# Kernel tuning notes

Measured on AMD Instinct MI355X. Metric: run time of the kernel, lower is better.

Reference implementation:

```python
import jax, jax.numpy as jnp
import numpy as np
from jax import lax

D = 256; NH = 8; LYR = 2; G = 64; K = G * G; T = 4; EC = 32
B = 4; N = 512; CITY = 256; DFF = 4 * D

def _conv(x, w):
    return lax.conv_general_dilated(x, w, (1, 1), 'SAME', dimension_numbers=('NCHW', 'OIHW', 'NCHW'))

def _ln(x, w, b):
    m = x.mean(-1, keepdims=True)
    v = ((x - m) ** 2).mean(-1, keepdims=True)
    return (x - m) / jnp.sqrt(v + 1e-5) * w + b

def _mlp(x, w1, b1, w2, b2):
    return jax.nn.gelu(x @ w1 + b1) @ w2 + b2

def setup_inputs():
    key = jax.random.key(0)
    ks = iter(jax.random.split(key, 64))
    def nrm(shape, s=0.02):
        return jax.random.normal(next(ks), shape, jnp.float32) * s
    return {
        'meas_xy': jax.random.uniform(next(ks), (B, N, 2), jnp.float32),
        'meas_v': jax.random.normal(next(ks), (B, N), jnp.float32),
        'bs_xy': jax.random.uniform(next(ks), (B, 1, 2), jnp.float32),
        'task_id': jax.random.randint(next(ks), (B,), 0, T),
        'city': jax.random.uniform(next(ks), (B, CITY, CITY), jnp.float32),
        'mp_w1': nrm((3, D)), 'mp_b1': jnp.zeros((D,)), 'mp_w2': nrm((D, D)), 'mp_b2': jnp.zeros((D,)),
        'bp_w1': nrm((2, D)), 'bp_b1': jnp.zeros((D,)), 'bp_w2': nrm((D, D)), 'bp_b2': jnp.zeros((D,)),
        'env_w1': nrm((EC, 1, 3, 3)), 'env_b1': jnp.zeros((EC,)),
        'env_w2': nrm((EC, EC, 3, 3)), 'env_b2': jnp.zeros((EC,)),
        'env_w3': nrm((D, EC, 1, 1)), 'env_b3': jnp.zeros((D,)),
        'task_emb': nrm((T, D)), 'tp_w': nrm((D, D)), 'tp_b': jnp.zeros((D,)),
        'grid_pos': nrm((K, D)),
        'blk_dens_w': nrm((LYR, D)), 'blk_dens_b': jnp.zeros((LYR, D)),
        'blk_ln1_w': jnp.ones((LYR, D)), 'blk_ln1_b': jnp.zeros((LYR, D)),
        'blk_wq': nrm((LYR, D, D)), 'blk_bq': jnp.zeros((LYR, D)),
        'blk_wk': nrm((LYR, D, D)), 'blk_bk': jnp.zeros((LYR, D)),
        'blk_wv': nrm((LYR, D, D)), 'blk_bv': jnp.zeros((LYR, D)),
        'blk_wo': nrm((LYR, D, D)), 'blk_bo': jnp.zeros((LYR, D)),
        'blk_ln2_w': jnp.ones((LYR, D)), 'blk_ln2_b': jnp.zeros((LYR, D)),
        'blk_ff_w1': nrm((LYR, D, DFF)), 'blk_ff_b1': jnp.zeros((LYR, DFF)),
        'blk_ff_w2': nrm((LYR, DFF, D)), 'blk_ff_b2': jnp.zeros((LYR, D)),
        'tfp_w': nrm((T, D, D)), 'tfp_b': jnp.zeros((T, D)),
        'head_w': nrm((D, 1)), 'head_b': jnp.zeros((1,)),
    }

def reference(meas_xy, meas_v, bs_xy, task_id, city, mp_w1, mp_b1, mp_w2, mp_b2, bp_w1, bp_b1, bp_w2, bp_b2, env_w1, env_b1, env_w2, env_b2, env_w3, env_b3, task_emb, tp_w, tp_b, grid_pos, blk_dens_w, blk_dens_b, blk_ln1_w, blk_ln1_b, blk_wq, blk_bq, blk_wk, blk_bk, blk_wv, blk_bv, blk_wo, blk_bo, blk_ln2_w, blk_ln2_b, blk_ff_w1, blk_ff_b1, blk_ff_w2, blk_ff_b2, tfp_w, tfp_b, head_w, head_b):
    b = meas_xy.shape[0]
    dh = D // NH
    # normalized grid cell centers, [K,2] in (x,y) order
    c = (jnp.arange(G, dtype=jnp.float32) + 0.5) / G
    gy, gx = jnp.meshgrid(c, c, indexing='ij')
    grid_xy = jnp.stack([gx, gy], -1).reshape(K, 2)
    meas_tok = _mlp(jnp.concatenate([meas_xy, meas_v[..., None]], -1), mp_w1, mp_b1, mp_w2, mp_b2)
    bs_tok = _mlp(bs_xy, bp_w1, bp_b1, bp_w2, bp_b2)
    src = jnp.concatenate([meas_tok, bs_tok], 1)       # [B,Ns,D]
    src_xy = jnp.concatenate([meas_xy, bs_xy], 1)      # [B,Ns,2]
    # distance bias: [B,K,Ns]
    attn_bias = -jnp.linalg.norm(grid_xy[None, :, None, :] - src_xy[:, None, :, :], axis=-1)
    # gaussian measurement density: [B,K]
    diff = grid_xy[None, :, None, :] - meas_xy[:, None, :, :]
    dist2 = (diff * diff).sum(-1)
    sigma = 0.08
    density = jnp.exp(-dist2 / (2.0 * sigma * sigma)).mean(-1)
    # env branch: nearest-resize city to GxG, small CNN
    idx = jnp.floor(jnp.arange(G) * (city.shape[1] / G)).astype(jnp.int32)
    city_grid = city[:, idx][:, :, idx][:, None]       # [B,1,G,G]
    h = jax.nn.gelu(_conv(city_grid, env_w1) + env_b1[None, :, None, None])
    h = jax.nn.gelu(_conv(h, env_w2) + env_b2[None, :, None, None])
    env_map = _conv(h, env_w3) + env_b3[None, :, None, None]
    env_grid = env_map.transpose(0, 2, 3, 1).reshape(b, K, D)
    task_vec = (task_emb[task_id] @ tp_w + tp_b)[:, None, :]
    grid = grid_pos[None] + task_vec + env_grid
    inv_sqrt = jnp.float32(1.0 / np.sqrt(dh))
    for l in range(LYR):
        # density modulation injected into the grid latent
        g = grid + density[..., None] * blk_dens_w[l] + blk_dens_b[l]
        hn = _ln(g, blk_ln1_w[l], blk_ln1_b[l])
        q = (hn @ blk_wq[l] + blk_bq[l]).reshape(b, K, NH, dh)
        kk = (src @ blk_wk[l] + blk_bk[l]).reshape(b, -1, NH, dh)
        vv = (src @ blk_wv[l] + blk_bv[l]).reshape(b, -1, NH, dh)
        scores = jnp.einsum('bkhd,bnhd->bhkn', q, kk) * inv_sqrt + attn_bias[:, None]
        a = jax.nn.softmax(scores, -1)
        o = jnp.einsum('bhkn,bnhd->bkhd', a, vv).reshape(b, K, D) @ blk_wo[l] + blk_bo[l]
        g = g + o
        g = g + _mlp(_ln(g, blk_ln2_w[l], blk_ln2_b[l]), blk_ff_w1[l], blk_ff_b1[l], blk_ff_w2[l], blk_ff_b2[l])
        grid = g
    # per-sample task projection from the weight bank
    tf = jax.nn.gelu(jnp.einsum('bkd,bdh->bkh', grid, tfp_w[task_id]) + tfp_b[task_id][:, None, :])
    logits = (tf @ head_w + head_b)[..., 0].reshape(b, G, G)
    return logits
```

## Files before the change

### kernel.cpp

```cpp
#include <hip/hip_runtime.h>
#include <hip/hip_bf16.h>
#include <math.h>

#define D 256
#define NH 8
#define DH 32
#define LYR 2
#define G 64
#define KK 4096
#define T 4
#define EC 32
#define B 4
#define N 512
#define CITY 256
#define DFF 1024
#define NS 513
#define NSP 544
#define MSRC 2052
#define MSRCP 2176
#define ISQ 0.17677669529663687f
#define LOG2E 1.4426950408889634f

typedef short bf16x8 __attribute__((ext_vector_type(8)));
typedef float f32x4 __attribute__((ext_vector_type(4)));

__device__ __forceinline__ float gelu_f(float x) {
    const float c2 = 2.f * 0.7978845608028654f * LOG2E;
    float u = x + 0.044715f * x * x * x;
    float e = __builtin_amdgcn_exp2f(-c2 * u);
    return x * __builtin_amdgcn_rcpf(1.f + e);
}

__device__ __forceinline__ unsigned short f2bf(float f) {
    unsigned int u = __float_as_uint(f);
    unsigned int r = (u + 0x7FFFu + ((u >> 16) & 1u)) >> 16;
    return (unsigned short)r;
}

__device__ __forceinline__ float bf2f(unsigned short u) {
    return __uint_as_float((unsigned)u << 16);
}

__device__ __forceinline__ unsigned cvtpk(float a, float b) {
    unsigned r;
    asm("v_cvt_pk_bf16_f32 %0, %1, %2" : "=v"(r) : "v"(a), "v"(b));
    return r;
}

__device__ __forceinline__ void gl2lds16(const unsigned short* g, unsigned short* l) {
    __builtin_amdgcn_global_load_lds(
        (const __attribute__((address_space(1))) unsigned int*)g,
        (__attribute__((address_space(3))) unsigned int*)l, 16, 0, 0);
}

__global__ __launch_bounds__(256) void pre1_k(
    const float* __restrict__ wq, const float* __restrict__ wk,
    const float* __restrict__ wv, const float* __restrict__ wo,
    const float* __restrict__ ff1, const float* __restrict__ ff2,
    const float* __restrict__ tfp,
    const float* __restrict__ bk, const float* __restrict__ bv,
    unsigned short* __restrict__ wqT, unsigned short* __restrict__ kvT,
    unsigned short* __restrict__ woT, unsigned short* __restrict__ ff1T,
    unsigned short* __restrict__ ff2T, unsigned short* __restrict__ tfpT,
    float* __restrict__ kvbias,
    const float* __restrict__ meas_xy, const float* __restrict__ meas_v,
    const float* __restrict__ bs_xy,
    const float* __restrict__ mp_w1, const float* __restrict__ mp_b1,
    const float* __restrict__ mp_w2, const float* __restrict__ mp_b2,
    const float* __restrict__ bp_w1, const float* __restrict__ bp_b1,
    const float* __restrict__ bp_w2, const float* __restrict__ bp_b2,
    unsigned short* __restrict__ srcbf, float* __restrict__ src_xy,
    float* __restrict__ dens,
    const float* __restrict__ city, const float* __restrict__ env_w1,
    const float* __restrict__ env_b1, float* __restrict__ h1,
    const float* __restrict__ task_emb, const int* __restrict__ task_id,
    const float* __restrict__ tp_w, const float* __restrict__ tp_b,
    float* __restrict__ tvec,
    unsigned short* __restrict__ khd, unsigned short* __restrict__ vch)
{
    __shared__ float sh[1088];
    int bx = blockIdx.x;
    int tid = threadIdx.x;
    if (bx < 1792) {
        const float* src; unsigned short* dst;
        int Kd, Nn, nmat, rowOff = 0, t; size_t matStride;
        if (bx < 512) {
            int job = bx >> 7; t = bx & 127;
            Kd = 256; Nn = 256; nmat = 2;
            if (job == 0)      { src = wq; dst = wqT; matStride = 65536; }
            else if (job == 1) { src = wk; dst = kvT; matStride = 131072; }
            else if (job == 2) { src = wv; dst = kvT; matStride = 131072; rowOff = 256; }
            else               { src = wo; dst = woT; matStride = 65536; }
            if ((t & 63) == 0 && job == 1) kvbias[(t >> 6) * 512 + tid] = bk[(t >> 6) * 256 + tid];
            if ((t & 63) == 0 && job == 2) kvbias[(t >> 6) * 512 + 256 + tid] = bv[(t >> 6) * 256 + tid];
        } else if (bx < 1024) { t = bx - 512;  src = ff1; dst = ff1T; Kd = 256;  Nn = 1024; nmat = 2; matStride = 262144; }
        else if (bx < 1536)   { t = bx - 1024; src = ff2; dst = ff2T; Kd = 1024; Nn = 256;  nmat = 2; matStride = 262144; }
        else                  { t = bx - 1536; src = tfp; dst = tfpT; Kd = 256;  Nn = 256;  nmat = 4; matStride = 65536; }
        int tn = Nn / 32, perMat = tn * (Kd / 32);
        int mat = t / perMat;
        int rem = t - mat * perMat;
        int nb = (rem % tn) * 32, kb = (rem / tn) * 32;
        const float* s = src + (size_t)mat * Kd * Nn;
        unsigned short* d = dst + (size_t)mat * matStride;
        float (*tb)[33] = (float (*)[33])sh;
        int tx = tid & 31, ty = tid >> 5;
        #pragma unroll
        for (int i = 0; i < 4; i++)
            tb[ty + i * 8][tx] = s[(size_t)(kb + ty + i * 8) * Nn + nb + tx];
        __syncthreads();
        #pragma unroll
        for (int i = 0; i < 4; i++)
            d[(size_t)(rowOff + nb + ty + i * 8) * Kd + kb + tx] = f2bf(tb[tx][ty + i * 8]);
    } else if (bx < 3968) {
        int id = bx - 1792;
        int dd = tid;
        if (id >= B * N + B) {
            srcbf[(size_t)id * D + dd] = 0;
            return;
        }
        float* hid = sh;
        int row;
        const float *w1, *b1, *w2, *b2;
        float x0, x1, x2 = 0.f;
        int nin;
        if (id < B * N) {
            int b = id >> 9, n = id & 511;
            x0 = meas_xy[(b * N + n) * 2 + 0];
            x1 = meas_xy[(b * N + n) * 2 + 1];
            x2 = meas_v[b * N + n];
            w1 = mp_w1; b1 = mp_b1; w2 = mp_w2; b2 = mp_b2; nin = 3;
            row = b * NS + n;
        } else {
            int b = id - B * N;
            x0 = bs_xy[b * 2 + 0];
            x1 = bs_xy[b * 2 + 1];
            w1 = bp_w1; b1 = bp_b1; w2 = bp_w2; b2 = bp_b2; nin = 2;
            row = b * NS + N;
        }
        float h = x0 * w1[dd] + x1 * w1[D + dd] + b1[dd];
        if (nin == 3) h += x2 * w1[2 * D + dd];
        hid[dd] = gelu_f(h);
        __syncthreads();
        float o = b2[dd];
        for (int j = 0; j < D; j++) o += hid[j] * w2[j * D + dd];
        srcbf[(size_t)row * D + dd] = f2bf(o);
        if (dd == 0) { src_xy[row * 2 + 0] = x0; src_xy[row * 2 + 1] = x1; }
    } else if (bx < 4032) {
        int blk = bx - 3968;
        int b = blk >> 4, kc = blk & 15;
        int k = kc * 256 + tid;
        float* mx = sh; float* my = sh + 512;
        for (int i = tid; i < N; i += 256) {
            mx[i] = meas_xy[(b * N + i) * 2 + 0];
            my[i] = meas_xy[(b * N + i) * 2 + 1];
        }
        __syncthreads();
        float gx = ((k & 63) + 0.5f) / 64.f;
        float gy = ((k >> 6) + 0.5f) / 64.f;
        float s = 0.f;
        for (int n = 0; n < N; n++) {
            float dx = gx - mx[n], dy = gy - my[n];
            s += __expf(-(dx * dx + dy * dy) * 78.125f);
        }
        dens[b * KK + k] = s * (1.f / (float)N);
    } else if (bx < 6080) {
        int i = (bx - 4032) * 256 + tid;
        int x = i & 63, y = (i >> 6) & 63, c = (i >> 12) & 31, b = i >> 17;
        float s = env_b1[c];
        for (int ky = 0; ky < 3; ky++) {
            int yy = y + ky - 1;
            if (yy < 0 || yy >= G) continue;
            for (int kx = 0; kx < 3; kx++) {
                int xx = x + kx - 1;
                if (xx < 0 || xx >= G) continue;
                s += city[(b * CITY + yy * 4) * CITY + xx * 4] * env_w1[c * 9 + ky * 3 + kx];
            }
        }
        h1[i] = gelu_f(s);
    } else if (bx < 6084) {
        int b = bx - 6080;
        float* e = sh;
        e[tid] = task_emb[task_id[b] * D + tid];
        __syncthreads();
        float s = tp_b[tid];
        for (int j = 0; j < D; j++) s += e[j] * tp_w[j * D + tid];
        tvec[b * D + tid] = s;
    } else {
        int bh = bx - 6084;
        unsigned short* kp = khd + ((size_t)bh * 544 + 513) * 32;
        for (int i = tid; i < 992; i += 256) kp[i] = 0;
        unsigned short* vp = vch + ((size_t)bh * 17 + 16) * 1024;
        for (int i = tid; i < 1024; i += 256) vp[i] = 0;
    }
}

__global__ __launch_bounds__(256) void conv2_k(
    const float* __restrict__ h1, const float* __restrict__ w,
    const float* __restrict__ bias, float* __restrict__ h2) {
    int blk = blockIdx.x;
    int yt = blk & 15, cg = (blk >> 4) & 7, b = blk >> 7;
    int x = threadIdx.x & 63, y = yt * 4 + (threadIdx.x >> 6);
    int c0 = cg * 4;
    float flag[9];
    int off[9];
    #pragma unroll
    for (int ky = 0; ky < 3; ky++) {
        int yy = y + ky - 1;
        bool vy = (yy >= 0 && yy < G);
        int yc = min(max(yy, 0), G - 1);
        #pragma unroll
        for (int kx = 0; kx < 3; kx++) {
            int xx = x + kx - 1;
            bool vx = (xx >= 0 && xx < G);
            int xc = min(max(xx, 0), G - 1);
            flag[ky * 3 + kx] = (vy && vx) ? 1.f : 0.f;
            off[ky * 3 + kx] = yc * G + xc;
        }
    }
    const float* hp = h1 + ((size_t)(b * EC) << 12);
    float acc[4] = {bias[c0], bias[c0 + 1], bias[c0 + 2], bias[c0 + 3]};
    float v[9], nv[9];
    #pragma unroll
    for (int t = 0; t < 9; t++) v[t] = hp[off[t]] * flag[t];
    for (int ci = 0; ci < EC; ci++) {
        if (ci < EC - 1) {
            const float* hn = hp + ((size_t)(ci + 1) << 12);
            #pragma unroll
            for (int t = 0; t < 9; t++) nv[t] = hn[off[t]] * flag[t];
        }
        #pragma unroll
        for (int cc = 0; cc < 4; cc++) {
            const float* wp = w + ((size_t)(c0 + cc) * EC + ci) * 9;
            #pragma unroll
            for (int t = 0; t < 9; t++) acc[cc] += v[t] * wp[t];
        }
        #pragma unroll
        for (int t = 0; t < 9; t++) v[t] = nv[t];
    }
    size_t obase = (((size_t)(b * EC + c0)) << 12) + y * G + x;
    #pragma unroll
    for (int cc = 0; cc < 4; cc++)
        h2[obase + ((size_t)cc << 12)] = gelu_f(acc[cc]);
}

__global__ __launch_bounds__(256) void pre2_k(
    const float* __restrict__ h2, const float* __restrict__ w3,
    const float* __restrict__ b3, const float* __restrict__ grid_pos,
    const float* __restrict__ tvec, float* __restrict__ grid,
    float* __restrict__ out, const float* __restrict__ head_b)
{
    __shared__ float sh[1088];
    int bx = blockIdx.x;
    int tid = threadIdx.x;
    if (bx < 2048) {
        int b = bx >> 9, k0 = (bx & 511) * 8;
        float (*h2s)[8] = (float (*)[8])sh;
        h2s[tid >> 3][tid & 7] = h2[(((size_t)b * EC + (tid >> 3)) << 12) + k0 + (tid & 7)];
        float w3r[32];
        #pragma unroll
        for (int c4 = 0; c4 < 8; c4++) {
            float4 w4 = *(const float4*)(w3 + tid * 32 + c4 * 4);
            w3r[c4 * 4 + 0] = w4.x; w3r[c4 * 4 + 1] = w4.y;
            w3r[c4 * 4 + 2] = w4.z; w3r[c4 * 4 + 3] = w4.w;
        }
        float base = b3[tid] + tvec[b * D + tid];
        __syncthreads();
        #pragma unroll
        for (int j = 0; j < 8; j++) {
            float s = base + grid_pos[(size_t)(k0 + j) * D + tid];
            #pragma unroll
            for (int ci = 0; ci < 32; ci++) s += h2s[ci][j] * w3r[ci];
            grid[((size_t)b * KK + k0 + j) * D + tid] = s;
        }
    } else {
        out[(bx - 2048) * 256 + tid] = head_b[0];
    }
}

template <int DENS>
__global__ __launch_bounds__(256) void dens_ln_k(
    float* __restrict__ grid, const float* __restrict__ dens,
    const float* __restrict__ dw, const float* __restrict__ db,
    const float* __restrict__ lw, const float* __restrict__ lb,
    unsigned short* __restrict__ y) {
    int row = blockIdx.x * 4 + (threadIdx.x >> 6);
    int lane = threadIdx.x & 63;
    float* gp = grid + (size_t)row * D + lane * 4;
    float4 v = *(float4*)gp;
    if (DENS) {
        float de = dens[row];
        float4 w4 = *(const float4*)(dw + lane * 4);
        float4 b4 = *(const float4*)(db + lane * 4);
        v.x += de * w4.x + b4.x; v.y += de * w4.y + b4.y;
        v.z += de * w4.z + b4.z; v.w += de * w4.w + b4.w;
        *(float4*)gp = v;
    }
    float s = v.x + v.y + v.z + v.w;
    #pragma unroll
    for (int o = 32; o > 0; o >>= 1) s += __shfl_xor(s, o);
    float mean = s * (1.f / D);
    float cx = v.x - mean, cy = v.y - mean, cz = v.z - mean, cw = v.w - mean;
    float q = cx * cx + cy * cy + cz * cz + cw * cw;
    #pragma unroll
    for (int o = 32; o > 0; o >>= 1) q += __shfl_xor(q, o);
    float inv = rsqrtf(q * (1.f / D) + 1e-5f);
    float4 lwv = *(const float4*)(lw + lane * 4);
    float4 lbv = *(const float4*)(lb + lane * 4);
    ushort4 o4;
    o4.x = f2bf(cx * inv * lwv.x + lbv.x);
    o4.y = f2bf(cy * inv * lwv.y + lbv.y);
    o4.z = f2bf(cz * inv * lwv.z + lbv.z);
    o4.w = f2bf(cw * inv * lwv.w + lbv.w);
    *(ushort4*)(y + (size_t)row * D + lane * 4) = o4;
}

template <int GELU, int ACCUM, int OBF, int TFPH, int STBF, int KVT = 0>
__device__ __forceinline__ void gemm_core(
    const unsigned short* __restrict__ A, const unsigned short* __restrict__ Wt,
    const float* __restrict__ bias, void* __restrict__ Cv,
    int M, int K, int Nn, int bn, int bm,
    const float* __restrict__ hw, unsigned short* __restrict__ Xb, float scale,
    unsigned short* As, unsigned short* Bs) {
    int tid = threadIdx.x;
    int wave = tid >> 6, lane = tid & 63;
    int q4 = lane >> 4, lr = lane & 15;
    int wn = wave * 16;
    int srow = tid >> 2;
    int sk8 = ((tid & 3) ^ ((tid >> 3) & 3)) * 8;
    const unsigned short* Ap  = A  + (size_t)(bm + srow) * K + sk8;
    const unsigned short* Bp0 = Wt + (size_t)(bn + srow) * K + sk8;
    unsigned short* AsD = As + tid * 8;
    unsigned short* BsD = Bs + tid * 8;
    int q4x = (q4 ^ ((lr >> 1) & 3)) * 8;
    f32x4 acc[4] = {};

    gl2lds16(Ap,       AsD);
    gl2lds16(Ap + 32,  AsD + 2048);
    gl2lds16(Bp0,      BsD);
    gl2lds16(Bp0 + 32, BsD + 2048);

    int nk = K >> 6;
    for (int ki = 0; ki < nk; ki++) {
        __syncthreads();
        if (ki + 1 < nk) {
            int k0 = (ki + 1) << 6;
            int nb = ((ki + 1) & 1) * 4096;
            gl2lds16(Ap + k0,       AsD + nb);
            gl2lds16(Ap + k0 + 32,  AsD + nb + 2048);
            gl2lds16(Bp0 + k0,      BsD + nb);
            gl2lds16(Bp0 + k0 + 32, BsD + nb + 2048);
        }
        int cb = (ki & 1) * 4096;
        #pragma unroll
        for (int ks = 0; ks < 2; ks++) {
            bf16x8 af[4], bf;
            #pragma unroll
            for (int i = 0; i < 4; i++)
                af[i] = *(const bf16x8*)&As[cb + ks * 2048 + (i * 16 + lr) * 32 + q4x];
            bf = *(const bf16x8*)&Bs[cb + ks * 2048 + (wn + lr) * 32 + q4x];
            #pragma unroll
            for (int i = 0; i < 4; i++)
                acc[i] = __builtin_amdgcn_mfma_f32_16x16x32_bf16(af[i], bf, acc[i], 0, 0, 0);
        }
    }

    if (KVT) {
        int gc = bn + wn + lr;
        float bv = bias[gc];
        bool isV = gc >= 256;
        #pragma unroll
        for (int i = 0; i < 4; i++) {
            #pragma unroll
            for (int r = 0; r < 4; r++) {
                int gr = bm + i * 16 + q4 * 4 + r;
                if (gr < MSRC) {
                    float v = acc[i][r] + bv;
                    int bb = gr / NS;
                    int tok = gr - bb * NS;
                    if (!isV) {
                        int h = gc >> 5, dh = gc & 31;
                        int t32 = tok & 31;
                        int kkp = ((t32 & 1) << 4) | ((t32 >> 3) << 2) | ((t32 >> 1) & 3);
                        int tokP = (tok & ~31) | kkp;
                        ((unsigned short*)Cv)[(((size_t)(bb * 8 + h) * 544) + tokP) * 32 + dh] = f2bf(v);
                    } else {
                        int gcv = gc - 256;
                        int h = gcv >> 5, dh = gcv & 31;
                        int c = tok >> 5, t32 = tok & 31;
                        Xb[((((size_t)(bb * 8 + h) * 17 + c) * 32 + dh)) * 32 + t32] = f2bf(v);
                    }
                }
            }
        }
        return;
    }

    if (TFPH) {
        int gc = bn + wn + lr;
        float bv = bias[gc];
        float hv = hw[gc];
        #pragma unroll
        for (int i = 0; i < 4; i++) {
            #pragma unroll
            for (int r = 0; r < 4; r++) {
                float s = gelu_f(acc[i][r] + bv) * hv;
                s += __shfl_xor(s, 1); s += __shfl_xor(s, 2);
                s += __shfl_xor(s, 4); s += __shfl_xor(s, 8);
                if (lr == 0)
                    atomicAdd((float*)Cv + (bm + i * 16 + q4 * 4 + r), s);
            }
        }
        return;
    }

    int gc = bn + wn + lr;
    float bv = bias[gc];
    #pragma unroll
    for (int i = 0; i < 4; i++) {
        #pragma unroll
        for (int r = 0; r < 4; r++) {
            int gr = bm + i * 16 + q4 * 4 + r;
            if (gr < M) {
                float v = (acc[i][r] + bv) * scale;
                if (GELU) v = gelu_f(v);
                size_t idx = (size_t)gr * Nn + gc;
                if (OBF) {
                    ((unsigned short*)Cv)[idx] = f2bf(v);
                } else if (ACCUM) {
                    float nv = ((float*)Cv)[idx] + v;
                    ((float*)Cv)[idx] = nv;
                    if (STBF) Xb[idx] = f2bf(nv);
                } else {
                    ((float*)Cv)[idx] = v;
                }
            }
        }
    }
}

template <int GELU, int ACCUM, int OBF, int TFPH, int STBF>
__global__ __launch_bounds__(256) void gemm_k(
    const unsigned short* __restrict__ A, const unsigned short* __restrict__ Wt0,
    const float* __restrict__ bias0, void* __restrict__ Cv,
    int M, int K, int Nn, const int* __restrict__ task_id,
    const float* __restrict__ hw, unsigned short* __restrict__ Xb) {
    __shared__ unsigned short As[8192];
    __shared__ unsigned short Bs[8192];
    const unsigned short* Wt = Wt0;
    const float* bias = bias0;
    int bm = blockIdx.y * 64;
    if (TFPH) { int t = task_id[bm >> 12]; Wt += (size_t)t * D * D; bias += t * D; }
    gemm_core<GELU, ACCUM, OBF, TFPH, STBF>(A, Wt, bias, Cv, M, K, Nn,
                                            blockIdx.x * 64, bm, hw, Xb, 1.f, As, Bs);
}

__global__ __launch_bounds__(256) void qkv_k(
    const unsigned short* __restrict__ xbf, const unsigned short* __restrict__ wqT,
    const float* __restrict__ bq, unsigned short* __restrict__ qbf,
    const unsigned short* __restrict__ srcbf, const unsigned short* __restrict__ kvT,
    const float* __restrict__ kvb, unsigned short* __restrict__ khd,
    unsigned short* __restrict__ vch) {
    __shared__ unsigned short As[8192];
    __shared__ unsigned short Bs[8192];
    if (blockIdx.x < 4) {
        gemm_core<0, 0, 1, 0, 0, 0>(xbf, wqT, bq, qbf, B * KK, D, D,
                                    blockIdx.x * 64, blockIdx.y * 64, nullptr, nullptr,
                                    ISQ * LOG2E, As, Bs);
    } else {
        if (blockIdx.y >= MSRCP / 64) return;
        gemm_core<0, 0, 1, 0, 0, 1>(srcbf, kvT, kvb, khd, MSRC, D, 512,
                                    (blockIdx.x - 4) * 64, blockIdx.y * 64, nullptr, vch, 1.f, As, Bs);
    }
}

__global__ __launch_bounds__(256) void attn_mfma(
    const unsigned short* __restrict__ qb,
    const unsigned short* __restrict__ khd,
    const unsigned short* __restrict__ vch,
    const float* __restrict__ sxy,
    unsigned short* __restrict__ out)
{
    __shared__ float2 sxys[NSP];
    int bid = blockIdx.x;
    int qt = bid & 63, h = (bid >> 6) & 7, b = bid >> 9;
    int tid = threadIdx.x, wave = tid >> 6, lane = tid & 63;
    int q4 = lane >> 4, lr = lane & 15;

    int kbase = qt * 64 + wave * 16;
    size_t qrow = (size_t)(b * KK + kbase + lr);
    bf16x8 qf = *(const bf16x8*)(qb + qrow * D + h * DH + q4 * 8);
    const unsigned short* kp0 = khd + ((size_t)(b * 8 + h) * 544) * 32 + lr * 32 + q4 * 8;
    const unsigned short* vb0 = vch + ((size_t)(b * 8 + h) * 17) * 1024 + lr * 32 + q4 * 8;

    float ll0 = 0.f, ll1 = 0.f;
    f32x4 o0 = {0.f, 0.f, 0.f, 0.f}, o1 = {0.f, 0.f, 0.f, 0.f};

    bf16x8 k0X, k1X, v0X, v1X, k0Y, k1Y, v0Y, v1Y;
    f32x4 d0X, d1X, d0Y, d1Y;

#define LDK(S, c) { size_t co = (size_t)(c) * 1024; \
    k0##S = *(const bf16x8*)(kp0 + co); k1##S = *(const bf16x8*)(kp0 + co + 512); }
#define LDV(S, c) { size_t co = (size_t)(c) * 1024; \
    v0##S = *(const bf16x8*)(vb0 + co); v1##S = *(const bf16x8*)(vb0 + co + 512); }

    LDK(X, 0); LDV(X, 0);
    LDK(Y, 1); LDV(Y, 1);

    const float2* sb = (const float2*)(sxy + 2 * (size_t)b * NS);
    for (int i = tid; i < NSP; i += 256)
        sxys[i] = (i < NS) ? sb[i] : make_float2(1.e4f, 1.e4f);
    __syncthreads();

    int qi = wave * 16 + lr;
    float gx = (qi + 0.5f) * (1.f / 64.f);
    float gy = (qt + 0.5f) * (1.f / 64.f);
    const float2* spf = &sxys[q4 * 8];

#define DIST(xx, yy) ({ float dx_ = gx - (xx), dy_ = gy - (yy); \
    __builtin_amdgcn_sqrtf(dx_ * dx_ + dy_ * dy_); })
#define LDB(S, c) { const float4* p4_ = (const float4*)(spf + (size_t)(c) * 32); \
    float4 a0_ = p4_[0], a1_ = p4_[1], a2_ = p4_[2], a3_ = p4_[3]; \
    d0##S[0] = DIST(a0_.x, a0_.y); d1##S[0] = DIST(a0_.z, a0_.w); \
    d0##S[1] = DIST(a1_.x, a1_.y); d1##S[1] = DIST(a1_.z, a1_.w); \
    d0##S[2] = DIST(a2_.x, a2_.y); d1##S[2] = DIST(a2_.z, a2_.w); \
    d0##S[3] = DIST(a3_.x, a3_.y); d1##S[3] = DIST(a3_.z, a3_.w); }

    LDB(X, 0); LDB(Y, 1);

#define BODY(S, cp) { \
    f32x4 s0 = {0.f, 0.f, 0.f, 0.f}, s1 = {0.f, 0.f, 0.f, 0.f}; \
    s0 = __builtin_amdgcn_mfma_f32_16x16x32_bf16(k0##S, qf, s0, 0, 0, 0); \
    s1 = __builtin_amdgcn_mfma_f32_16x16x32_bf16(k1##S, qf, s1, 0, 0, 0); \
    LDK(S, cp); \
    float p0[4], p1[4]; \
    p0[0] = __builtin_amdgcn_exp2f(__builtin_fmaf(d0##S[0], -LOG2E, s0[0])); \
    p0[1] = __builtin_amdgcn_exp2f(__builtin_fmaf(d0##S[1], -LOG2E, s0[1])); \
    p0[2] = __builtin_amdgcn_exp2f(__builtin_fmaf(d0##S[2], -LOG2E, s0[2])); \
    p0[3] = __builtin_amdgcn_exp2f(__builtin_fmaf(d0##S[3], -LOG2E, s0[3])); \
    p1[0] = __builtin_amdgcn_exp2f(__builtin_fmaf(d1##S[0], -LOG2E, s1[0])); \
    p1[1] = __builtin_amdgcn_exp2f(__builtin_fmaf(d1##S[1], -LOG2E, s1[1])); \
    p1[2] = __builtin_amdgcn_exp2f(__builtin_fmaf(d1##S[2], -LOG2E, s1[2])); \
    p1[3] = __builtin_amdgcn_exp2f(__builtin_fmaf(d1##S[3], -LOG2E, s1[3])); \
    LDB(S, cp); \
    ll0 += (p0[0] + p0[1]) + (p0[2] + p0[3]); \
    ll1 += (p1[0] + p1[1]) + (p1[2] + p1[3]); \
    union { unsigned u[4]; bf16x8 v; } pu; \
    pu.u[0] = cvtpk(p0[0], p1[0]); \
    pu.u[1] = cvtpk(p0[1], p1[1]); \
    pu.u[2] = cvtpk(p0[2], p1[2]); \
    pu.u[3] = cvtpk(p0[3], p1[3]); \
    o0 = __builtin_amdgcn_mfma_f32_16x16x32_bf16(v0##S, pu.v, o0, 0, 0, 0); \
    o1 = __builtin_amdgcn_mfma_f32_16x16x32_bf16(v1##S, pu.v, o1, 0, 0, 0); \
    LDV(S, cp); \
}

    for (int c = 0; c < 16; c += 2) {
        int cpX = c + 2;
        int cpY = (c + 3 > 16) ? 16 : c + 3;
        BODY(X, cpX);
        BODY(Y, cpY);
    }
    BODY(X, 16);

#undef BODY
#undef LDB
#undef DIST
#undef LDK
#undef LDV

    float ll = ll0 + ll1;
    ll += __shfl_xor(ll, 16);
    ll += __shfl_xor(ll, 32);
    float inv = 1.f / ll;
    unsigned w0 = cvtpk(o0[0] * inv, o0[1] * inv);
    unsigned w1 = cvtpk(o0[2] * inv, o0[3] * inv);
    unsigned w2 = cvtpk(o1[0] * inv, o1[1] * inv);
    unsigned w3 = cvtpk(o1[2] * inv, o1[3] * inv);
    uint2 st0; st0.x = w0; st0.y = w1;
    uint2 st1; st1.x = w2; st1.y = w3;
    *(uint2*)(out + qrow * D + h * DH + q4 * 4) = st0;
    *(uint2*)(out + qrow * D + h * DH + 16 + q4 * 4) = st1;
}

extern "C" void kernel_launch(void* const* d_in, const int* in_sizes, int n_in,
                              void* d_out, int out_size, void* d_ws, size_t ws_size,
                              hipStream_t stream) {
    const float* meas_xy = (const float*)d_in[0];
    const float* meas_v  = (const float*)d_in[1];
    const float* bs_xy   = (const float*)d_in[2];
    const int*   task_id = (const int*)d_in[3];
    const float* city    = (const float*)d_in[4];
    const float* mp_w1 = (const float*)d_in[5];  const float* mp_b1 = (const float*)d_in[6];
    const float* mp_w2 = (const float*)d_in[7];  const float* mp_b2 = (const float*)d_in[8];
    const float* bp_w1 = (const float*)d_in[9];  const float* bp_b1 = (const float*)d_in[10];
    const float* bp_w2 = (const float*)d_in[11]; const float* bp_b2 = (const float*)d_in[12];
    const float* env_w1 = (const float*)d_in[13]; const float* env_b1 = (const float*)d_in[14];
    const float* env_w2 = (const float*)d_in[15]; const float* env_b2 = (const float*)d_in[16];
    const float* env_w3 = (const float*)d_in[17]; const float* env_b3 = (const float*)d_in[18];
    const float* task_emb = (const float*)d_in[19];
    const float* tp_w = (const float*)d_in[20]; const float* tp_b = (const float*)d_in[21];
    const float* grid_pos = (const float*)d_in[22];
    const float* dens_w = (const float*)d_in[23]; const float* dens_b = (const float*)d_in[24];
    const float* ln1_w = (const float*)d_in[25]; const float* ln1_b = (const float*)d_in[26];
    const float* wq = (const float*)d_in[27]; const float* bq = (const float*)d_in[28];
    const float* wk = (const float*)d_in[29]; const float* bk = (const float*)d_in[30];
    const float* wv = (const float*)d_in[31]; const float* bv = (const float*)d_in[32];
    const float* wo = (const float*)d_in[33]; const float* bo = (const float*)d_in[34];
    const float* ln2_w = (const float*)d_in[35]; const float* ln2_b = (const float*)d_in[36];
    const float* ff_w1 = (const float*)d_in[37]; const float* ff_b1 = (const float*)d_in[38];
    const float* ff_w2 = (const float*)d_in[39]; const float* ff_b2 = (const float*)d_in[40];
    const float* tfp_w = (const float*)d_in[41]; const float* tfp_b = (const float*)d_in[42];
    const float* head_w = (const float*)d_in[43]; const float* head_b = (const float*)d_in[44];
    float* out = (float*)d_out;

    float* ws = (float*)d_ws;
    size_t off = 0;
    float* src_xy = ws + off; off += (size_t)B * NS * 2 + 128;
    float* dens   = ws + off; off += (size_t)B * KK;
    float* tvec   = ws + off; off += (size_t)B * D;
    float* h1     = ws + off; off += (size_t)B * EC * KK;
    float* grid   = ws + off; off += (size_t)B * KK * D;
    unsigned short* srcbf = (unsigned short*)(ws + off); off += (size_t)MSRCP * D / 2;
    unsigned short* khd   = (unsigned short*)(ws + off); off += (size_t)B * 8 * 544 * 32 / 2;
    unsigned short* vch   = (unsigned short*)(ws + off); off += (size_t)B * 8 * 17 * 1024 / 2;
    float* qreg   = ws + off; off += (size_t)B * KK * D / 2;
    unsigned short* qbf = (unsigned short*)qreg;
    float* h2     = qreg;
    unsigned short* xbf    = (unsigned short*)(ws + off); off += (size_t)B * KK * D / 2;
    unsigned short* attnbf = (unsigned short*)(ws + off); off += (size_t)B * KK * D / 2;
    unsigned short* hidbf  = (unsigned short*)(ws + off); off += (size_t)B * KK * DFF / 2;
    unsigned short* wqT  = (unsigned short*)(ws + off); off += (size_t)LYR * D * D / 2;
    unsigned short* kvT  = (unsigned short*)(ws + off); off += (size_t)LYR * 512 * D / 2;
    unsigned short* woT  = (unsigned short*)(ws + off); off += (size_t)LYR * D * D / 2;
    unsigned short* ff1T = (unsigned short*)(ws + off); off += (size_t)LYR * D * DFF / 2;
    unsigned short* ff2T = (unsigned short*)(ws + off); off += (size_t)LYR * DFF * D / 2;
    unsigned short* tfpT = (unsigned short*)(ws + off); off += (size_t)T * D * D / 2;
    float* kvbias = ws + off; off += (size_t)LYR * 512;
    (void)ws_size; (void)n_in; (void)in_sizes; (void)out_size;

    const int M = B * KK;

    pre1_k<<<6116, 256, 0, stream>>>(
        wq, wk, wv, wo, ff_w1, ff_w2, tfp_w, bk, bv,
        wqT, kvT, woT, ff1T, ff2T, tfpT, kvbias,
        meas_xy, meas_v, bs_xy, mp_w1, mp_b1, mp_w2, mp_b2,
        bp_w1, bp_b1, bp_w2, bp_b2, srcbf, src_xy,
        dens, city, env_w1, env_b1, h1,
        task_emb, task_id, tp_w, tp_b, tvec, khd, vch);
    conv2_k<<<512, 256, 0, stream>>>(h1, env_w2, env_b2, h2);
    pre2_k<<<2112, 256, 0, stream>>>(h2, env_w3, env_b3, grid_pos, tvec, grid,
                                     out, head_b);

    for (int l = 0; l < LYR; l++) {
        dens_ln_k<1><<<M / 4, 256, 0, stream>>>(grid, dens, dens_w + l * D, dens_b + l * D,
                                                ln1_w + l * D, ln1_b + l * D, xbf);
        qkv_k<<<dim3(12, 256), 256, 0, stream>>>(
            xbf, wqT + (size_t)l * D * D, bq + l * D, qbf,
            srcbf, kvT + (size_t)l * 512 * D, kvbias + l * 512, khd, vch);
        attn_mfma<<<B * NH * 64, 256, 0, stream>>>(qbf, khd, vch, src_xy, attnbf);
        gemm_k<0, 1, 0, 0, 0><<<dim3(4, 256), 256, 0, stream>>>(
            attnbf, woT + (size_t)l * D * D, bo + l * D, grid, M, D, D, nullptr, nullptr, nullptr);
        dens_ln_k<0><<<M / 4, 256, 0, stream>>>(grid, nullptr, nullptr, nullptr,
                                                ln2_w + l * D, ln2_b + l * D, xbf);
        gemm_k<1, 0, 1, 0, 0><<<dim3(16, 256), 256, 0, stream>>>(
            xbf, ff1T + (size_t)l * D * DFF, ff_b1 + l * DFF, hidbf, M, D, DFF,
            nullptr, nullptr, nullptr);
        if (l == 0) {
            gemm_k<0, 1, 0, 0, 0><<<dim3(4, 256), 256, 0, stream>>>(
                hidbf, ff2T + (size_t)l * DFF * D, ff_b2 + l * D, grid, M, DFF, D,
                nullptr, nullptr, nullptr);
        } else {
            gemm_k<0, 1, 0, 0, 1><<<dim3(4, 256), 256, 0, stream>>>(
                hidbf, ff2T + (size_t)l * DFF * D, ff_b2 + l * D, grid, M, DFF, D,
                nullptr, nullptr, xbf);
        }
    }
    gemm_k<1, 0, 0, 1, 0><<<dim3(4, 256), 256, 0, stream>>>(
        xbf, tfpT, tfp_b, out, M, D, D, task_id, head_w, nullptr);
}
```

Measured before the change: 536.7 us.

## Process two heads per attention block, sharing distance-bias computation

Each attention block now handles two heads instead of one, halving the grid size. The distance bias (sqrt and coordinate setup) is computed once and reused for both heads. The LOG2E scaling and the y-distance term are folded into the shared-memory preprocessing, so each bias costs one fma plus a sqrt. In exchange the kernel uses more registers and launches fewer blocks, which may reduce occupancy and latency hiding.

```diff
diff --git a/kernel.cpp b/kernel.cpp
--- a/kernel.cpp
+++ b/kernel.cpp
@@ -482,42 +482,53 @@
 {
     __shared__ float2 sxys[NSP];
     int bid = blockIdx.x;
-    int qt = bid & 63, h = (bid >> 6) & 7, b = bid >> 9;
+    int qt = bid & 63, h2 = (bid >> 6) & 3, b = bid >> 8;
+    int ha = h2 * 2, hb = ha + 1;
     int tid = threadIdx.x, wave = tid >> 6, lane = tid & 63;
     int q4 = lane >> 4, lr = lane & 15;
 
     int kbase = qt * 64 + wave * 16;
     size_t qrow = (size_t)(b * KK + kbase + lr);
-    bf16x8 qf = *(const bf16x8*)(qb + qrow * D + h * DH + q4 * 8);
-    const unsigned short* kp0 = khd + ((size_t)(b * 8 + h) * 544) * 32 + lr * 32 + q4 * 8;
-    const unsigned short* vb0 = vch + ((size_t)(b * 8 + h) * 17) * 1024 + lr * 32 + q4 * 8;
-
-    float ll0 = 0.f, ll1 = 0.f;
-    f32x4 o0 = {0.f, 0.f, 0.f, 0.f}, o1 = {0.f, 0.f, 0.f, 0.f};
-
-    bf16x8 k0X, k1X, v0X, v1X, k0Y, k1Y, v0Y, v1Y;
+    bf16x8 qfA = *(const bf16x8*)(qb + qrow * D + ha * DH + q4 * 8);
+    bf16x8 qfB = *(const bf16x8*)(qb + qrow * D + hb * DH + q4 * 8);
+    const unsigned short* kpA = khd + ((size_t)(b * 8 + ha) * 544) * 32 + lr * 32 + q4 * 8;
+    const unsigned short* kpB = khd + ((size_t)(b * 8 + hb) * 544) * 32 + lr * 32 + q4 * 8;
+    const unsigned short* vbA = vch + ((size_t)(b * 8 + ha) * 17) * 1024 + lr * 32 + q4 * 8;
+    const unsigned short* vbB = vch + ((size_t)(b * 8 + hb) * 17) * 1024 + lr * 32 + q4 * 8;
+
+    float lla0 = 0.f, lla1 = 0.f, llb0 = 0.f, llb1 = 0.f;
+    f32x4 o0a = {0.f, 0.f, 0.f, 0.f}, o1a = {0.f, 0.f, 0.f, 0.f};
+    f32x4 o0b = {0.f, 0.f, 0.f, 0.f}, o1b = {0.f, 0.f, 0.f, 0.f};
+
+    bf16x8 ka0X, ka1X, kb0X, kb1X, va0X, va1X, vb0X, vb1X;
+    bf16x8 ka0Y, ka1Y, kb0Y, kb1Y, va0Y, va1Y, vb0Y, vb1Y;
     f32x4 d0X, d1X, d0Y, d1Y;
 
 #define LDK(S, c) { size_t co = (size_t)(c) * 1024; \
-    k0##S = *(const bf16x8*)(kp0 + co); k1##S = *(const bf16x8*)(kp0 + co + 512); }
+    ka0##S = *(const bf16x8*)(kpA + co); ka1##S = *(const bf16x8*)(kpA + co + 512); \
+    kb0##S = *(const bf16x8*)(kpB + co); kb1##S = *(const bf16x8*)(kpB + co + 512); }
 #define LDV(S, c) { size_t co = (size_t)(c) * 1024; \
-    v0##S = *(const bf16x8*)(vb0 + co); v1##S = *(const bf16x8*)(vb0 + co + 512); }
+    va0##S = *(const bf16x8*)(vbA + co); va1##S = *(const bf16x8*)(vbA + co + 512); \
+    vb0##S = *(const bf16x8*)(vbB + co); vb1##S = *(const bf16x8*)(vbB + co + 512); }
 
     LDK(X, 0); LDV(X, 0);
     LDK(Y, 1); LDV(Y, 1);
 
+    float gy = (qt + 0.5f) * (1.f / 64.f);
     const float2* sb = (const float2*)(sxy + 2 * (size_t)b * NS);
-    for (int i = tid; i < NSP; i += 256)
-        sxys[i] = (i < NS) ? sb[i] : make_float2(1.e4f, 1.e4f);
+    for (int i = tid; i < NSP; i += 256) {
+        float2 v = (i < NS) ? sb[i] : make_float2(1.e4f, 1.e4f);
+        float ey = (gy - v.y) * LOG2E;
+        sxys[i] = make_float2(v.x * LOG2E, ey * ey);
+    }
     __syncthreads();
 
     int qi = wave * 16 + lr;
-    float gx = (qi + 0.5f) * (1.f / 64.f);
-    float gy = (qt + 0.5f) * (1.f / 64.f);
+    float gxp = (qi + 0.5f) * (1.f / 64.f) * LOG2E;
     const float2* spf = &sxys[q4 * 8];
 
-#define DIST(xx, yy) ({ float dx_ = gx - (xx), dy_ = gy - (yy); \
-    __builtin_amdgcn_sqrtf(dx_ * dx_ + dy_ * dy_); })
+#define DIST(xx, yy2) ({ float dx_ = gxp - (xx); \
+    __builtin_amdgcn_sqrtf(__builtin_fmaf(dx_, dx_, (yy2))); })
 #define LDB(S, c) { const float4* p4_ = (const float4*)(spf + (size_t)(c) * 32); \
     float4 a0_ = p4_[0], a1_ = p4_[1], a2_ = p4_[2], a3_ = p4_[3]; \
     d0##S[0] = DIST(a0_.x, a0_.y); d1##S[0] = DIST(a0_.z, a0_.w); \
@@ -528,29 +539,48 @@
     LDB(X, 0); LDB(Y, 1);
 
 #define BODY(S, cp) { \
-    f32x4 s0 = {0.f, 0.f, 0.f, 0.f}, s1 = {0.f, 0.f, 0.f, 0.f}; \
-    s0 = __builtin_amdgcn_mfma_f32_16x16x32_bf16(k0##S, qf, s0, 0, 0, 0); \
-    s1 = __builtin_amdgcn_mfma_f32_16x16x32_bf16(k1##S, qf, s1, 0, 0, 0); \
+    f32x4 s0a = {0.f, 0.f, 0.f, 0.f}, s1a = {0.f, 0.f, 0.f, 0.f}; \
+    f32x4 s0b = {0.f, 0.f, 0.f, 0.f}, s1b = {0.f, 0.f, 0.f, 0.f}; \
+    s0a = __builtin_amdgcn_mfma_f32_16x16x32_bf16(ka0##S, qfA, s0a, 0, 0, 0); \
+    s1a = __builtin_amdgcn_mfma_f32_16x16x32_bf16(ka1##S, qfA, s1a, 0, 0, 0); \
+    s0b = __builtin_amdgcn_mfma_f32_16x16x32_bf16(kb0##S, qfB, s0b, 0, 0, 0); \
+    s1b = __builtin_amdgcn_mfma_f32_16x16x32_bf16(kb1##S, qfB, s1b, 0, 0, 0); \
     LDK(S, cp); \
-    float p0[4], p1[4]; \
-    p0[0] = __builtin_amdgcn_exp2f(__builtin_fmaf(d0##S[0], -LOG2E, s0[0])); \
-    p0[1] = __builtin_amdgcn_exp2f(__builtin_fmaf(d0##S[1], -LOG2E, s0[1])); \
-    p0[2] = __builtin_amdgcn_exp2f(__builtin_fmaf(d0##S[2], -LOG2E, s0[2])); \
-    p0[3] = __builtin_amdgcn_exp2f(__builtin_fmaf(d0##S[3], -LOG2E, s0[3])); \
-    p1[0] = __builtin_amdgcn_exp2f(__builtin_fmaf(d1##S[0], -LOG2E, s1[0])); \
-    p1[1] = __builtin_amdgcn_exp2f(__builtin_fmaf(d1##S[1], -LOG2E, s1[1])); \
-    p1[2] = __builtin_amdgcn_exp2f(__builtin_fmaf(d1##S[2], -LOG2E, s1[2])); \
-    p1[3] = __builtin_amdgcn_exp2f(__builtin_fmaf(d1##S[3], -LOG2E, s1[3])); \
+    float p0a[4], p1a[4], p0b[4], p1b[4]; \
+    p0a[0] = __builtin_amdgcn_exp2f(s0a[0] - d0##S[0]); \
+    p0a[1] = __builtin_amdgcn_exp2f(s0a[1] - d0##S[1]); \
+    p0a[2] = __builtin_amdgcn_exp2f(s0a[2] - d0##S[2]); \
+    p0a[3] = __builtin_amdgcn_exp2f(s0a[3] - d0##S[3]); \
+    p1a[0] = __builtin_amdgcn_exp2f(s1a[0] - d1##S[0]); \
+    p1a[1] = __builtin_amdgcn_exp2f(s1a[1] - d1##S[1]); \
+    p1a[2] = __builtin_amdgcn_exp2f(s1a[2] - d1##S[2]); \
+    p1a[3] = __builtin_amdgcn_exp2f(s1a[3] - d1##S[3]); \
+    p0b[0] = __builtin_amdgcn_exp2f(s0b[0] - d0##S[0]); \
+    p0b[1] = __builtin_amdgcn_exp2f(s0b[1] - d0##S[1]); \
+    p0b[2] = __builtin_amdgcn_exp2f(s0b[2] - d0##S[2]); \
+    p0b[3] = __builtin_amdgcn_exp2f(s0b[3] - d0##S[3]); \
+    p1b[0] = __builtin_amdgcn_exp2f(s1b[0] - d1##S[0]); \
+    p1b[1] = __builtin_amdgcn_exp2f(s1b[1] - d1##S[1]); \
+    p1b[2] = __builtin_amdgcn_exp2f(s1b[2] - d1##S[2]); \
+    p1b[3] = __builtin_amdgcn_exp2f(s1b[3] - d1##S[3]); \
     LDB(S, cp); \
-    ll0 += (p0[0] + p0[1]) + (p0[2] + p0[3]); \
-    ll1 += (p1[0] + p1[1]) + (p1[2] + p1[3]); \
-    union { unsigned u[4]; bf16x8 v; } pu; \
-    pu.u[0] = cvtpk(p0[0], p1[0]); \
-    pu.u[1] = cvtpk(p0[1], p1[1]); \
-    pu.u[2] = cvtpk(p0[2], p1[2]); \
-    pu.u[3] = cvtpk(p0[3], p1[3]); \
-    o0 = __builtin_amdgcn_mfma_f32_16x16x32_bf16(v0##S, pu.v, o0, 0, 0, 0); \
-    o1 = __builtin_amdgcn_mfma_f32_16x16x32_bf16(v1##S, pu.v, o1, 0, 0, 0); \
+    lla0 += (p0a[0] + p0a[1]) + (p0a[2] + p0a[3]); \
+    lla1 += (p1a[0] + p1a[1]) + (p1a[2] + p1a[3]); \
+    llb0 += (p0b[0] + p0b[1]) + (p0b[2] + p0b[3]); \
+    llb1 += (p1b[0] + p1b[1]) + (p1b[2] + p1b[3]); \
+    union { unsigned u[4]; bf16x8 v; } pua, pub; \
+    pua.u[0] = cvtpk(p0a[0], p1a[0]); \
+    pua.u[1] = cvtpk(p0a[1], p1a[1]); \
+    pua.u[2] = cvtpk(p0a[2], p1a[2]); \
+    pua.u[3] = cvtpk(p0a[3], p1a[3]); \
+    pub.u[0] = cvtpk(p0b[0], p1b[0]); \
+    pub.u[1] = cvtpk(p0b[1], p1b[1]); \
+    pub.u[2] = cvtpk(p0b[2], p1b[2]); \
+    pub.u[3] = cvtpk(p0b[3], p1b[3]); \
+    o0a = __builtin_amdgcn_mfma_f32_16x16x32_bf16(va0##S, pua.v, o0a, 0, 0, 0); \
+    o1a = __builtin_amdgcn_mfma_f32_16x16x32_bf16(va1##S, pua.v, o1a, 0, 0, 0); \
+    o0b = __builtin_amdgcn_mfma_f32_16x16x32_bf16(vb0##S, pub.v, o0b, 0, 0, 0); \
+    o1b = __builtin_amdgcn_mfma_f32_16x16x32_bf16(vb1##S, pub.v, o1b, 0, 0, 0); \
     LDV(S, cp); \
 }
 
@@ -568,18 +598,27 @@
 #undef LDK
 #undef LDV
 
-    float ll = ll0 + ll1;
-    ll += __shfl_xor(ll, 16);
-    ll += __shfl_xor(ll, 32);
-    float inv = 1.f / ll;
-    unsigned w0 = cvtpk(o0[0] * inv, o0[1] * inv);
-    unsigned w1 = cvtpk(o0[2] * inv, o0[3] * inv);
-    unsigned w2 = cvtpk(o1[0] * inv, o1[1] * inv);
-    unsigned w3 = cvtpk(o1[2] * inv, o1[3] * inv);
-    uint2 st0; st0.x = w0; st0.y = w1;
-    uint2 st1; st1.x = w2; st1.y = w3;
-    *(uint2*)(out + qrow * D + h * DH + q4 * 4) = st0;
-    *(uint2*)(out + qrow * D + h * DH + 16 + q4 * 4) = st1;
+    float lla = lla0 + lla1;
+    lla += __shfl_xor(lla, 16);
+    lla += __shfl_xor(lla, 32);
+    float inva = 1.f / lla;
+    float llb = llb0 + llb1;
+    llb += __shfl_xor(llb, 16);
+    llb += __shfl_xor(llb, 32);
+    float invb = 1.f / llb;
+    uint2 sa0, sa1, sb0, sb1;
+    sa0.x = cvtpk(o0a[0] * inva, o0a[1] * inva);
+    sa0.y = cvtpk(o0a[2] * inva, o0a[3] * inva);
+    sa1.x = cvtpk(o1a[0] * inva, o1a[1] * inva);
+    sa1.y = cvtpk(o1a[2] * inva, o1a[3] * inva);
+    sb0.x = cvtpk(o0b[0] * invb, o0b[1] * invb);
+    sb0.y = cvtpk(o0b[2] * invb, o0b[3] * invb);
+    sb1.x = cvtpk(o1b[0] * invb, o1b[1] * invb);
+    sb1.y = cvtpk(o1b[2] * invb, o1b[3] * invb);
+    *(uint2*)(out + qrow * D + ha * DH + q4 * 4) = sa0;
+    *(uint2*)(out + qrow * D + ha * DH + 16 + q4 * 4) = sa1;
+    *(uint2*)(out + qrow * D + hb * DH + q4 * 4) = sb0;
+    *(uint2*)(out + qrow * D + hb * DH + 16 + q4 * 4) = sb1;
 }
 
 extern "C" void kernel_launch(void* const* d_in, const int* in_sizes, int n_in,
@@ -657,7 +696,7 @@
         qkv_k<<<dim3(12, 256), 256, 0, stream>>>(
             xbf, wqT + (size_t)l * D * D, bq + l * D, qbf,
             srcbf, kvT + (size_t)l * 512 * D, kvbias + l * 512, khd, vch);
-        attn_mfma<<<B * NH * 64, 256, 0, stream>>>(qbf, khd, vch, src_xy, attnbf);
+        attn_mfma<<<B * 4 * 64, 256, 0, stream>>>(qbf, khd, vch, src_xy, attnbf);
         gemm_k<0, 1, 0, 0, 0><<<dim3(4, 256), 256, 0, stream>>>(
             attnbf, woT + (size_t)l * D * D, bo + l * D, grid, M, D, D, nullptr, nullptr, nullptr);
         dens_ln_k<0><<<M / 4, 256, 0, stream>>>(grid, nullptr, nullptr, nullptr,
```

After: 544.1 us. Within noise of the previous version (+1.4%).

## Add 128-row GEMM tile for FFN/output projections and prescale attention distance bias

Applied to the files above, without the earlier changes.

Adds a gemm128_k kernel that computes a 128x64 output tile per block, with each wave holding eight MFMA accumulators. It replaces the 64x64 gemm_k for the output projection and both FFN GEMMs. Each B fragment is reused across eight A fragments, which lowers LDS and global traffic per FLOP, at the cost of more registers, twice the LDS for A, and half as many blocks. In attention, source coordinates are pre-scaled by LOG2E and the y-distance term is precomputed into shared memory, which removes a subtract, a multiply and an FMA per score in the inner loop.

```diff
diff --git a/kernel.cpp b/kernel.cpp
--- a/kernel.cpp
+++ b/kernel.cpp
@@ -454,6 +454,84 @@
                                             blockIdx.x * 64, bm, hw, Xb, 1.f, As, Bs);
 }
 
+template <int GELU, int ACCUM, int OBF, int STBF>
+__global__ __launch_bounds__(256) void gemm128_k(
+    const unsigned short* __restrict__ A, const unsigned short* __restrict__ Wt,
+    const float* __restrict__ bias, void* __restrict__ Cv,
+    int M, int K, int Nn, unsigned short* __restrict__ Xb) {
+    __shared__ unsigned short As[16384];
+    __shared__ unsigned short Bs[8192];
+    int tid = threadIdx.x;
+    int wave = tid >> 6, lane = tid & 63;
+    int q4 = lane >> 4, lr = lane & 15;
+    int wn = wave * 16;
+    int bn = blockIdx.x * 64, bm = blockIdx.y * 128;
+    int srow = tid >> 2;
+    int sk8 = ((tid & 3) ^ ((tid >> 3) & 3)) * 8;
+    const unsigned short* Ap  = A + (size_t)(bm + srow) * K + sk8;
+    const unsigned short* Ap2 = Ap + (size_t)64 * K;
+    const unsigned short* Bp  = Wt + (size_t)(bn + srow) * K + sk8;
+    unsigned short* AsD = As + tid * 8;
+    unsigned short* BsD = Bs + tid * 8;
+    int q4x = (q4 ^ ((lr >> 1) & 3)) * 8;
+    f32x4 acc[8] = {};
+
+    gl2lds16(Ap,        AsD);
+    gl2lds16(Ap2,       AsD + 2048);
+    gl2lds16(Ap + 32,   AsD + 4096);
+    gl2lds16(Ap2 + 32,  AsD + 6144);
+    gl2lds16(Bp,        BsD);
+    gl2lds16(Bp + 32,   BsD + 2048);
+
+    int nk = K >> 6;
+    for (int ki = 0; ki < nk; ki++) {
+        __syncthreads();
+        if (ki + 1 < nk) {
+            int k0 = (ki + 1) << 6;
+            int nbA = ((ki + 1) & 1) * 8192;
+            int nbB = ((ki + 1) & 1) * 4096;
+            gl2lds16(Ap + k0,        AsD + nbA);
+            gl2lds16(Ap2 + k0,       AsD + nbA + 2048);
+            gl2lds16(Ap + k0 + 32,   AsD + nbA + 4096);
+            gl2lds16(Ap2 + k0 + 32,  AsD + nbA + 6144);
+            gl2lds16(Bp + k0,        BsD + nbB);
+            gl2lds16(Bp + k0 + 32,   BsD + nbB + 2048);
+        }
+        int cbA = (ki & 1) * 8192, cbB = (ki & 1) * 4096;
+        #pragma unroll
+        for (int ks = 0; ks < 2; ks++) {
+            bf16x8 bf = *(const bf16x8*)&Bs[cbB + ks * 2048 + (wn + lr) * 32 + q4x];
+            #pragma unroll
+            for (int i = 0; i < 8; i++) {
+                bf16x8 af = *(const bf16x8*)&As[cbA + ks * 4096 + (i * 16 + lr) * 32 + q4x];
+                acc[i] = __builtin_amdgcn_mfma_f32_16x16x32_bf16(af, bf, acc[i], 0, 0, 0);
+            }
+        }
+    }
+
+    int gc = bn + wn + lr;
+    float bv = bias[gc];
+    #pragma unroll
+    for (int i = 0; i < 8; i++) {
+        #pragma unroll
+        for (int r = 0; r < 4; r++) {
+            int gr = bm + i * 16 + q4 * 4 + r;
+            float v = acc[i][r] + bv;
+            if (GELU) v = gelu_f(v);
+            size_t idx = (size_t)gr * Nn + gc;
+            if (OBF) {
+                ((unsigned short*)Cv)[idx] = f2bf(v);
+            } else if (ACCUM) {
+                float nv = ((float*)Cv)[idx] + v;
+                ((float*)Cv)[idx] = nv;
+                if (STBF) Xb[idx] = f2bf(nv);
+            } else {
+                ((float*)Cv)[idx] = v;
+            }
+        }
+    }
+}
+
 __global__ __launch_bounds__(256) void qkv_k(
     const unsigned short* __restrict__ xbf, const unsigned short* __restrict__ wqT,
     const float* __restrict__ bq, unsigned short* __restrict__ qbf,
@@ -506,18 +584,21 @@
     LDK(X, 0); LDV(X, 0);
     LDK(Y, 1); LDV(Y, 1);
 
+    float gy = (qt + 0.5f) * (1.f / 64.f);
     const float2* sb = (const float2*)(sxy + 2 * (size_t)b * NS);
-    for (int i = tid; i < NSP; i += 256)
-        sxys[i] = (i < NS) ? sb[i] : make_float2(1.e4f, 1.e4f);
+    for (int i = tid; i < NSP; i += 256) {
+        float2 v = (i < NS) ? sb[i] : make_float2(1.e4f, 1.e4f);
+        float ey = (gy - v.y) * LOG2E;
+        sxys[i] = make_float2(v.x * LOG2E, ey * ey);
+    }
     __syncthreads();
 
     int qi = wave * 16 + lr;
-    float gx = (qi + 0.5f) * (1.f / 64.f);
-    float gy = (qt + 0.5f) * (1.f / 64.f);
+    float gxp = (qi + 0.5f) * (1.f / 64.f) * LOG2E;
     const float2* spf = &sxys[q4 * 8];
 
-#define DIST(xx, yy) ({ float dx_ = gx - (xx), dy_ = gy - (yy); \
-    __builtin_amdgcn_sqrtf(dx_ * dx_ + dy_ * dy_); })
+#define DIST(xx, yy2) ({ float dx_ = gxp - (xx); \
+    __builtin_amdgcn_sqrtf(__builtin_fmaf(dx_, dx_, (yy2))); })
 #define LDB(S, c) { const float4* p4_ = (const float4*)(spf + (size_t)(c) * 32); \
     float4 a0_ = p4_[0], a1_ = p4_[1], a2_ = p4_[2], a3_ = p4_[3]; \
     d0##S[0] = DIST(a0_.x, a0_.y); d1##S[0] = DIST(a0_.z, a0_.w); \
@@ -533,14 +614,14 @@
     s1 = __builtin_amdgcn_mfma_f32_16x16x32_bf16(k1##S, qf, s1, 0, 0, 0); \
     LDK(S, cp); \
     float p0[4], p1[4]; \
-    p0[0] = __builtin_amdgcn_exp2f(__builtin_fmaf(d0##S[0], -LOG2E, s0[0])); \
-    p0[1] = __builtin_amdgcn_exp2f(__builtin_fmaf(d0##S[1], -LOG2E, s0[1])); \
-    p0[2] = __builtin_amdgcn_exp2f(__builtin_fmaf(d0##S[2], -LOG2E, s0[2])); \
-    p0[3] = __builtin_amdgcn_exp2f(__builtin_fmaf(d0##S[3], -LOG2E, s0[3])); \
-    p1[0] = __builtin_amdgcn_exp2f(__builtin_fmaf(d1##S[0], -LOG2E, s1[0])); \
-    p1[1] = __builtin_amdgcn_exp2f(__builtin_fmaf(d1##S[1], -LOG2E, s1[1])); \
-    p1[2] = __builtin_amdgcn_exp2f(__builtin_fmaf(d1##S[2], -LOG2E, s1[2])); \
-    p1[3] = __builtin_amdgcn_exp2f(__builtin_fmaf(d1##S[3], -LOG2E, s1[3])); \
+    p0[0] = __builtin_amdgcn_exp2f(s0[0] - d0##S[0]); \
+    p0[1] = __builtin_amdgcn_exp2f(s0[1] - d0##S[1]); \
+    p0[2] = __builtin_amdgcn_exp2f(s0[2] - d0##S[2]); \
+    p0[3] = __builtin_amdgcn_exp2f(s0[3] - d0##S[3]); \
+    p1[0] = __builtin_amdgcn_exp2f(s1[0] - d1##S[0]); \
+    p1[1] = __builtin_amdgcn_exp2f(s1[1] - d1##S[1]); \
+    p1[2] = __builtin_amdgcn_exp2f(s1[2] - d1##S[2]); \
+    p1[3] = __builtin_amdgcn_exp2f(s1[3] - d1##S[3]); \
     LDB(S, cp); \
     ll0 += (p0[0] + p0[1]) + (p0[2] + p0[3]); \
     ll1 += (p1[0] + p1[1]) + (p1[2] + p1[3]); \
@@ -658,21 +739,18 @@
             xbf, wqT + (size_t)l * D * D, bq + l * D, qbf,
             srcbf, kvT + (size_t)l * 512 * D, kvbias + l * 512, khd, vch);
         attn_mfma<<<B * NH * 64, 256, 0, stream>>>(qbf, khd, vch, src_xy, attnbf);
-        gemm_k<0, 1, 0, 0, 0><<<dim3(4, 256), 256, 0, stream>>>(
-            attnbf, woT + (size_t)l * D * D, bo + l * D, grid, M, D, D, nullptr, nullptr, nullptr);
+        gemm128_k<0, 1, 0, 0><<<dim3(4, 128), 256, 0, stream>>>(
+            attnbf, woT + (size_t)l * D * D, bo + l * D, grid, M, D, D, nullptr);
         dens_ln_k<0><<<M / 4, 256, 0, stream>>>(grid, nullptr, nullptr, nullptr,
                                                 ln2_w + l * D, ln2_b + l * D, xbf);
-        gemm_k<1, 0, 1, 0, 0><<<dim3(16, 256), 256, 0, stream>>>(
-            xbf, ff1T + (size_t)l * D * DFF, ff_b1 + l * DFF, hidbf, M, D, DFF,
-            nullptr, nullptr, nullptr);
+        gemm128_k<1, 0, 1, 0><<<dim3(16, 128), 256, 0, stream>>>(
+            xbf, ff1T + (size_t)l * D * DFF, ff_b1 + l * DFF, hidbf, M, D, DFF, nullptr);
         if (l == 0) {
-            gemm_k<0, 1, 0, 0, 0><<<dim3(4, 256), 256, 0, stream>>>(
-                hidbf, ff2T + (size_t)l * DFF * D, ff_b2 + l * D, grid, M, DFF, D,
-                nullptr, nullptr, nullptr);
+            gemm128_k<0, 1, 0, 0><<<dim3(4, 128), 256, 0, stream>>>(
+                hidbf, ff2T + (size_t)l * DFF * D, ff_b2 + l * D, grid, M, DFF, D, nullptr);
         } else {
-            gemm_k<0, 1, 0, 0, 1><<<dim3(4, 256), 256, 0, stream>>>(
-                hidbf, ff2T + (size_t)l * DFF * D, ff_b2 + l * D, grid, M, DFF, D,
-                nullptr, nullptr, xbf);
+            gemm128_k<0, 1, 0, 1><<<dim3(4, 128), 256, 0, stream>>>(
+                hidbf, ff2T + (size_t)l * DFF * D, ff_b2 + l * D, grid, M, DFF, D, xbf);
         }
     }
     gemm_k<1, 0, 0, 1, 0><<<dim3(4, 256), 256, 0, stream>>>(
```

Result: no change. 531.5 us (-1.0%).
